# Kernel optimization log

Hardware: AMD Instinct MI355X
Metric: run time of the kernel (lower is better)

The kernel has to match this reference:

```python
import jax, jax.numpy as jnp
import numpy as np
import math

DIM = 1024
N_HEADS = 16
HEAD_DIM = DIM // N_HEADS


def get_sin_cos(seq_len, dim):
    # theta: (dim/2,), freqs: (L, dim/2), emb: (L, dim)
    theta = 10000.0 ** (-jnp.arange(0, dim, 2, dtype=jnp.float32) / dim)
    position = jnp.arange(seq_len, dtype=jnp.float32)
    freqs = position[:, None] * theta[None, :]
    emb = jnp.concatenate([jnp.sin(freqs), jnp.cos(freqs)], axis=-1)
    sin = emb[None, None]  # (1,1,L,dim)
    cos = emb[None, None]
    return sin, cos


def rotate_half(x):
    x1, x2 = x[..., ::2], x[..., 1::2]
    return jnp.concatenate([-x2, x1], axis=-1)


def apply_rope(q, k):
    sin, cos = get_sin_cos(q.shape[2], q.shape[-1])
    q = q * cos + rotate_half(q) * sin
    k = k * cos + rotate_half(k) * sin
    return q, k


def setup_inputs() -> dict:
    key = jax.random.key(0)
    ks = jax.random.split(key, 3)
    B, L, D = 2, 2048, DIM
    x = jax.random.normal(ks[0], (B, L, D), dtype=jnp.float32)
    Wqkv = jax.random.normal(ks[1], (D, 3 * D), dtype=jnp.float32) * (1.0 / math.sqrt(D))
    bqkv = jnp.zeros((3 * D,), dtype=jnp.float32)
    Wout = jax.random.normal(ks[2], (D, D), dtype=jnp.float32) * (1.0 / math.sqrt(D))
    bout = jnp.zeros((D,), dtype=jnp.float32)
    return {"x": x, "Wqkv": Wqkv, "bqkv": bqkv, "Wout": Wout, "bout": bout}


def reference(x, Wqkv, bqkv, Wout, bout):
    B, L, D = x.shape
    H, Hd = N_HEADS, HEAD_DIM
    qkv = (x @ Wqkv + bqkv).reshape(B, L, 3, H, Hd)
    q, k, v = qkv[:, :, 0], qkv[:, :, 1], qkv[:, :, 2]  # (B,L,H,Hd)
    q = q.transpose(0, 2, 1, 3)  # (B,H,L,Hd)
    k = k.transpose(0, 2, 1, 3)
    v = v.transpose(0, 2, 1, 3)
    q, k = apply_rope(q, k)
    scores = jnp.einsum('bhqd,bhkd->bhqk', q, k) / math.sqrt(Hd)
    probs = jax.nn.softmax(scores, axis=-1)
    out = jnp.einsum('bhqk,bhkd->bhqd', probs, v)
    out = out.transpose(0, 2, 1, 3).reshape(B, L, D)
    return out @ Wout + bout
```

## Files before the change

### kernel.cpp

```cpp
#include <hip/hip_runtime.h>
#include <hip/hip_bf16.h>
#include <math.h>

typedef __bf16 bf16;
typedef __bf16 bf16x8 __attribute__((ext_vector_type(8)));
typedef __bf16 bf16x4 __attribute__((ext_vector_type(4)));
typedef float f32x4 __attribute__((ext_vector_type(4)));
typedef float f32x16 __attribute__((ext_vector_type(16)));

#define DEV __device__ __forceinline__
#define AS1(p) ((const __attribute__((address_space(1))) void*)(p))
#define AS3(p) ((__attribute__((address_space(3))) void*)(p))

#define Bsz 2
#define Lseq 2048
#define Dm 1024
#define Hh 16
#define HD 64
#define BL (Bsz * Lseq)
#define TN (3 * Dm)

#define LOG2E 1.44269504088896f

#define OFF_XATT  ((size_t)0)
#define OFF_WQKVT (OFF_XATT  + (size_t)BL * Dm * 2)
#define OFF_WOUTT (OFF_WQKVT + (size_t)TN * Dm * 2)
#define OFF_TAB   (OFF_WOUTT + (size_t)Dm * Dm * 2)
#define OFF_Q     (OFF_TAB   + (size_t)Lseq * 32 * 8)
#define OFF_K     (OFF_Q     + (size_t)BL * Dm * 2)
#define OFF_VT    (OFF_K     + (size_t)BL * Dm * 2)

DEV float exp2_fast(float x) {
    float r;
    asm("v_exp_f32 %0, %1" : "=v"(r) : "v"(x));
    return r;
}

__global__ __launch_bounds__(256) void k_convert(const float* __restrict__ in,
                                                 bf16* __restrict__ out) {
    int i = blockIdx.x * 256 + threadIdx.x;
    const float4* in4 = (const float4*)in;
    float4 a = in4[i * 2];
    float4 b = in4[i * 2 + 1];
    bf16x8 o;
    o[0] = (bf16)a.x; o[1] = (bf16)a.y; o[2] = (bf16)a.z; o[3] = (bf16)a.w;
    o[4] = (bf16)b.x; o[5] = (bf16)b.y; o[6] = (bf16)b.z; o[7] = (bf16)b.w;
    ((bf16x8*)out)[i] = o;
}

__global__ __launch_bounds__(256) void k_transpose(const float* __restrict__ in,
                                                   bf16* __restrict__ out,
                                                   int R, int C) {
    __shared__ float t[32][33];
    int bx = blockIdx.x * 32;
    int by = blockIdx.y * 32;
    int tx = threadIdx.x, ty = threadIdx.y;
#pragma unroll
    for (int i = 0; i < 32; i += 8)
        t[ty + i][tx] = in[(size_t)(by + ty + i) * C + bx + tx];
    __syncthreads();
#pragma unroll
    for (int i = 0; i < 32; i += 8)
        out[(size_t)(bx + ty + i) * R + by + tx] = (bf16)t[tx][ty + i];
}

__global__ __launch_bounds__(256) void k_sincos(float2* __restrict__ tab) {
    int idx = blockIdx.x * 256 + threadIdx.x;
    int pos = idx >> 5, t = idx & 31;
    float theta = powf(10000.0f, -(float)t * (1.0f / 32.0f));
    float f = (float)pos * theta;
    tab[idx] = make_float2(sinf(f), cosf(f));
}

template <int EPI>
DEV void gemm_body(const bf16* __restrict__ A,
                   const bf16* __restrict__ BT,
                   const float* __restrict__ bias,
                   float* __restrict__ C,
                   bf16* __restrict__ qo,
                   bf16* __restrict__ ko,
                   bf16* __restrict__ vt,
                   const float2* __restrict__ tab,
                   int N, int K) {
    __shared__ uint4 smem4[2048];
    char* Al = (char*)smem4;
    char* Bl = (char*)smem4 + 16384;
    const int tid = threadIdx.x;
    const int w = tid >> 6, lane = tid & 63, lg = lane >> 4, lr = lane & 15;
    const int m0 = blockIdx.y * 128, n0 = blockIdx.x * 128;
    const int wm = (w >> 1) * 64, wn = (w & 1) * 64;
    const char* Ab = (const char*)A;
    const char* Bb = (const char*)BT;
    const size_t Kb = (size_t)K * 2;

    f32x4 acc[4][4] = {};

    const int rowL = lane >> 3;
    const int j16 = ((lane & 7) ^ rowL) * 16;

    for (int kt = 0; kt < K; kt += 64) {
#pragma unroll
        for (int c = 0; c < 4; ++c) {
            const int R0 = (w * 4 + c) * 8;
            const int row = R0 + rowL;
            __builtin_amdgcn_global_load_lds(AS1(Ab + (size_t)(m0 + row) * Kb + kt * 2 + j16),
                                             AS3(Al + R0 * 128), 16, 0, 0);
            __builtin_amdgcn_global_load_lds(AS1(Bb + (size_t)(n0 + row) * Kb + kt * 2 + j16),
                                             AS3(Bl + R0 * 128), 16, 0, 0);
        }
        __syncthreads();
#pragma unroll
        for (int kf = 0; kf < 2; ++kf) {
            bf16x8 af[4], bfr[4];
#pragma unroll
            for (int i = 0; i < 4; ++i) {
                int ra = wm + i * 16 + lr;
                af[i] = *(const bf16x8*)(Al + ra * 128 + ((kf * 64 + lg * 16) ^ ((ra & 7) << 4)));
                int rb = wn + i * 16 + lr;
                bfr[i] = *(const bf16x8*)(Bl + rb * 128 + ((kf * 64 + lg * 16) ^ ((rb & 7) << 4)));
            }
#pragma unroll
            for (int i = 0; i < 4; ++i)
#pragma unroll
                for (int j = 0; j < 4; ++j)
                    acc[i][j] = __builtin_amdgcn_mfma_f32_16x16x32_bf16(af[i], bfr[j], acc[i][j], 0, 0, 0);
        }
        __syncthreads();
    }

    if constexpr (EPI == 0) {
#pragma unroll
        for (int i = 0; i < 4; ++i) {
            int row = m0 + wm + i * 16 + lg * 4;
#pragma unroll
            for (int j = 0; j < 4; ++j) {
                int col = n0 + wn + j * 16 + lr;
                float bv = bias[col];
#pragma unroll
                for (int r = 0; r < 4; ++r)
                    C[(size_t)(row + r) * N + col] = acc[i][j][r] + bv;
            }
        }
    } else {
        const int phase = n0 >> 10;
        const int c0 = n0 + wn;
        const int h = (c0 & 1023) >> 6;
        const int b = m0 >> 11;
        const int bh = b * 16 + h;
        const int lbase = (m0 & 2047) + wm;
        float bv[4];
#pragma unroll
        for (int j = 0; j < 4; ++j) bv[j] = bias[c0 + j * 16 + lr];
        float* Lw = (float*)((char*)smem4 + w * 4096);

#pragma unroll
        for (int i = 0; i < 4; ++i) {
#pragma unroll
            for (int j = 0; j < 4; ++j)
#pragma unroll
                for (int r = 0; r < 4; ++r)
                    Lw[(lg * 4 + r) * 64 + j * 16 + lr] = acc[i][j][r] + bv[j];
            __syncthreads();
            if (phase < 2) {
                const float scale = (phase == 0) ? 0.125f * LOG2E : 1.0f;
                bf16* dst = (phase == 0 ? qo : ko) + (size_t)bh * Lseq * 64;
#pragma unroll
                for (int j = 0; j < 4; ++j)
#pragma unroll
                    for (int r = 0; r < 4; ++r) {
                        int rl = lg * 4 + r;
                        int d = j * 16 + lr;
                        int l = lbase + i * 16 + rl;
                        float v = Lw[rl * 64 + d];
                        int dp = (d < 32) ? (2 * d + 1) : (2 * d - 64);
                        float p = Lw[rl * 64 + dp];
                        float2 f = tab[l * 32 + (d & 31)];
                        float val = ((d < 32) ? (v - p) * f.x : (v + p) * f.y) * scale;
                        dst[(size_t)l * 64 + d] = (bf16)val;
                    }
            } else {
                int d = lane;
                int lb = lbase + i * 16;
                bf16x8 o1, o2;
#pragma unroll
                for (int rw = 0; rw < 8; ++rw) {
                    o1[rw] = (bf16)Lw[rw * 64 + d];
                    o2[rw] = (bf16)Lw[(rw + 8) * 64 + d];
                }
                bf16* dst = vt + ((size_t)bh * 64 + d) * Lseq + lb;
                *(bf16x8*)dst = o1;
                *(bf16x8*)(dst + 8) = o2;
            }
            __syncthreads();
        }
    }
}

__global__ __launch_bounds__(256) void k_gemm_qkv(const bf16* __restrict__ A,
                                                  const bf16* __restrict__ BT,
                                                  const float* __restrict__ bias,
                                                  bf16* __restrict__ qo,
                                                  bf16* __restrict__ ko,
                                                  bf16* __restrict__ vt,
                                                  const float2* __restrict__ tab) {
    gemm_body<1>(A, BT, bias, nullptr, qo, ko, vt, tab, TN, Dm);
}
__global__ __launch_bounds__(256) void k_gemm_out(const bf16* __restrict__ A,
                                                  const bf16* __restrict__ BT,
                                                  const float* __restrict__ bias,
                                                  float* __restrict__ C) {
    gemm_body<0>(A, BT, bias, C, nullptr, nullptr, nullptr, nullptr, Dm, Dm);
}

DEV f32x16 mfma32(bf16x8 a, bf16x8 b, f32x16 c) {
    return __builtin_amdgcn_mfma_f32_32x32x16_bf16(a, b, c, 0, 0, 0);
}
DEV unsigned packbf(float lo, float hi) {
    unsigned short a = __builtin_bit_cast(unsigned short, (bf16)lo);
    unsigned short b = __builtin_bit_cast(unsigned short, (bf16)hi);
    return (unsigned)a | ((unsigned)b << 16);
}

DEV void stage_tile(const char* kb, const char* vb, char* Kn, char* Vn,
                    int j0, int w, int lane) {
#pragma unroll
    for (int c = 0; c < 2; ++c) {
        const int j = w * 2 + c;
        const int rsw = lane ^ j;
        __builtin_amdgcn_global_load_lds(AS1(kb + (size_t)(j0 + rsw) * 128 + j * 16),
                                         AS3(Kn + j * 1024), 16, 0, 0);
        __builtin_amdgcn_global_load_lds(AS1(vb + (size_t)rsw * 4096 + (size_t)j0 * 2 + j * 16),
                                         AS3(Vn + j * 1024), 16, 0, 0);
    }
}

__global__ __launch_bounds__(256, 2) void k_attn(const bf16* __restrict__ Q,
                                                 const bf16* __restrict__ Kt,
                                                 const bf16* __restrict__ Vt,
                                                 bf16* __restrict__ Op) {
    __shared__ uint4 smem4[2048];
    char* base = (char*)smem4;
    const int tid = threadIdx.x;
    const int w = tid >> 6, lane = tid & 63;
    const int hi = lane >> 5, l31 = lane & 31;
    const int bid = blockIdx.x;
    const int bh = bid >> 4, qt = bid & 15;
    const int q0 = qt * 128 + w * 32;
    const char* qb = (const char*)(Q + (size_t)bh * Lseq * 64);
    const char* kb = (const char*)(Kt + (size_t)bh * Lseq * 64);
    const char* vb = (const char*)(Vt + (size_t)bh * 64 * Lseq);

    bf16x8 qf[4];
#pragma unroll
    for (int kst = 0; kst < 4; ++kst)
        qf[kst] = *(const bf16x8*)(qb + (size_t)(q0 + l31) * 128 + kst * 32 + hi * 16);

    f32x16 o0 = {}, o1 = {};
    float m = -1e30f, lsum = 0.f;

    stage_tile(kb, vb, base, base + 8192, 0, w, lane);
    __syncthreads();

    for (int jt = 0; jt < 32; ++jt) {
        const int cur = jt & 1;
        const char* Kl = base + cur * 16384;
        const char* Vl = Kl + 8192;
        char* Kn = base + (cur ^ 1) * 16384;
        char* Vn = Kn + 8192;

        if (jt < 31) stage_tile(kb, vb, Kn, Vn, (jt + 1) * 64, w, lane);

        f32x16 s0 = {}, s1 = {};
        __builtin_amdgcn_s_setprio(1);
#pragma unroll
        for (int kst = 0; kst < 4; ++kst) {
            const int jK = kst * 2 + hi;
            const int x = l31 ^ jK;
            bf16x8 ka = *(const bf16x8*)(Kl + jK * 1024 + x * 16);
            bf16x8 kc = *(const bf16x8*)(Kl + jK * 1024 + (32 + x) * 16);
            s0 = mfma32(ka, qf[kst], s0);
            s1 = mfma32(kc, qf[kst], s1);
        }
        __builtin_amdgcn_s_setprio(0);

        float pm = fmaxf(s0[0], s0[1]);
#pragma unroll
        for (int r = 2; r < 16; ++r) pm = fmaxf(pm, s0[r]);
#pragma unroll
        for (int r = 0; r < 16; ++r) pm = fmaxf(pm, s1[r]);
        pm = fmaxf(pm, __shfl_xor(pm, 32));
        if (!__all(pm <= m + 8.0f)) {
            float mn = fmaxf(m, pm);
            float sc = exp2_fast(m - mn);
#pragma unroll
            for (int r = 0; r < 16; ++r) { o0[r] *= sc; o1[r] *= sc; }
            lsum *= sc; m = mn;
        }
        float rs = 0.f;
#pragma unroll
        for (int r = 0; r < 16; ++r) { s0[r] = exp2_fast(s0[r] - m); rs += s0[r]; }
#pragma unroll
        for (int r = 0; r < 16; ++r) { s1[r] = exp2_fast(s1[r] - m); rs += s1[r]; }
        rs += __shfl_xor(rs, 32);
        lsum += rs;

        unsigned u[16];
#pragma unroll
        for (int t = 0; t < 8; ++t) {
            u[t]     = packbf(s0[2 * t], s0[2 * t + 1]);
            u[8 + t] = packbf(s1[2 * t], s1[2 * t + 1]);
        }
        unsigned snd[8], rcv[8];
#pragma unroll
        for (int J = 0; J < 2; ++J)
#pragma unroll
            for (int st = 0; st < 2; ++st) {
                const int t0 = J * 8 + st * 4, q = (J * 2 + st) * 2;
                snd[q + 0] = hi ? u[t0 + 0] : u[t0 + 2];
                snd[q + 1] = hi ? u[t0 + 1] : u[t0 + 3];
            }
#pragma unroll
        for (int t = 0; t < 8; ++t) rcv[t] = __shfl_xor(snd[t], 32);
        bf16x8 pf[2][2];
#pragma unroll
        for (int J = 0; J < 2; ++J)
#pragma unroll
            for (int st = 0; st < 2; ++st) {
                const int t0 = J * 8 + st * 4, q = (J * 2 + st) * 2;
                union { unsigned wd[4]; bf16x8 v; } f;
                f.wd[0] = hi ? rcv[q + 0] : u[t0 + 0];
                f.wd[1] = hi ? rcv[q + 1] : u[t0 + 1];
                f.wd[2] = hi ? u[t0 + 2] : rcv[q + 0];
                f.wd[3] = hi ? u[t0 + 3] : rcv[q + 1];
                pf[J][st] = f.v;
            }

        __builtin_amdgcn_s_setprio(1);
#pragma unroll
        for (int J = 0; J < 2; ++J)
#pragma unroll
            for (int st = 0; st < 2; ++st) {
                const int jV = J * 4 + st * 2 + hi;
                const int x = l31 ^ jV;
                bf16x8 v0 = *(const bf16x8*)(Vl + jV * 1024 + x * 16);
                bf16x8 v1 = *(const bf16x8*)(Vl + jV * 1024 + (32 + x) * 16);
                o0 = mfma32(v0, pf[J][st], o0);
                o1 = mfma32(v1, pf[J][st], o1);
            }
        __builtin_amdgcn_s_setprio(0);
        __syncthreads();
    }

    const float inv = 1.0f / lsum;
    const int b = bh >> 4, h = bh & 15;
    bf16* dst = Op + (size_t)(b * Lseq + q0 + l31) * Dm + h * 64;
#pragma unroll
    for (int t = 0; t < 4; ++t) {
        bf16x4 p0, p1;
#pragma unroll
        for (int i = 0; i < 4; ++i) {
            p0[i] = (bf16)(o0[4 * t + i] * inv);
            p1[i] = (bf16)(o1[4 * t + i] * inv);
        }
        *(bf16x4*)(dst + 8 * t + 4 * hi) = p0;
        *(bf16x4*)(dst + 32 + 8 * t + 4 * hi) = p1;
    }
}

extern "C" void kernel_launch(void* const* d_in, const int* in_sizes, int n_in,
                              void* d_out, int out_size, void* d_ws, size_t ws_size,
                              hipStream_t stream) {
    (void)in_sizes; (void)n_in; (void)out_size; (void)ws_size;
    const float* x    = (const float*)d_in[0];
    const float* Wqkv = (const float*)d_in[1];
    const float* bqkv = (const float*)d_in[2];
    const float* Wout = (const float*)d_in[3];
    const float* bout = (const float*)d_in[4];
    float* out = (float*)d_out;
    char* ws = (char*)d_ws;

    bf16* xbf    = (bf16*)(ws + OFF_XATT);
    bf16* att    = (bf16*)(ws + OFF_XATT);
    bf16* wqkvT  = (bf16*)(ws + OFF_WQKVT);
    bf16* woutT  = (bf16*)(ws + OFF_WOUTT);
    float2* tab  = (float2*)(ws + OFF_TAB);
    bf16* qb     = (bf16*)(ws + OFF_Q);
    bf16* kb     = (bf16*)(ws + OFF_K);
    bf16* vt     = (bf16*)(ws + OFF_VT);

    hipLaunchKernelGGL(k_convert, dim3((BL * Dm) / 8 / 256), dim3(256), 0, stream, x, xbf);
    hipLaunchKernelGGL(k_transpose, dim3(TN / 32, Dm / 32), dim3(32, 8), 0, stream, Wqkv, wqkvT, Dm, TN);
    hipLaunchKernelGGL(k_transpose, dim3(Dm / 32, Dm / 32), dim3(32, 8), 0, stream, Wout, woutT, Dm, Dm);
    hipLaunchKernelGGL(k_sincos, dim3(Lseq * 32 / 256), dim3(256), 0, stream, tab);
    hipLaunchKernelGGL(k_gemm_qkv, dim3(TN / 128, BL / 128), dim3(256), 0, stream,
                       xbf, wqkvT, bqkv, qb, kb, vt, tab);
    hipLaunchKernelGGL(k_attn, dim3(32 * 16), dim3(256), 0, stream, qb, kb, vt, att);
    hipLaunchKernelGGL(k_gemm_out, dim3(Dm / 128, BL / 128), dim3(256), 0, stream,
                       att, woutT, bout, out);
}
```

Before: 144.1 us.

## Split attention KV range across two wave groups per block and merge softmax

The attention block grows to 512 threads. Two sets of four waves each process half of the key/value sequence for the same 128 queries, and each set has its own double-buffered LDS region. At the end the partial outputs, maxima and sums are exchanged through LDS and merged flash-decoding style. This doubles the waves available to hide latency and halves the serial loop length per wave. The cost is doubled LDS use, a final reduction step, and fewer resident blocks per CU.

```diff
diff --git a/kernel.cpp b/kernel.cpp
--- a/kernel.cpp
+++ b/kernel.cpp
@@ -222,10 +222,10 @@
 }
 
 DEV void stage_tile(const char* kb, const char* vb, char* Kn, char* Vn,
-                    int j0, int w, int lane) {
+                    int j0, int qw, int lane) {
 #pragma unroll
     for (int c = 0; c < 2; ++c) {
-        const int j = w * 2 + c;
+        const int j = qw * 2 + c;
         const int rsw = lane ^ j;
         __builtin_amdgcn_global_load_lds(AS1(kb + (size_t)(j0 + rsw) * 128 + j * 16),
                                          AS3(Kn + j * 1024), 16, 0, 0);
@@ -234,21 +234,23 @@
     }
 }
 
-__global__ __launch_bounds__(256, 2) void k_attn(const bf16* __restrict__ Q,
+__global__ __launch_bounds__(512, 4) void k_attn(const bf16* __restrict__ Q,
                                                  const bf16* __restrict__ Kt,
                                                  const bf16* __restrict__ Vt,
                                                  bf16* __restrict__ Op) {
-    __shared__ uint4 smem4[2048];
+    __shared__ uint4 smem4[4096];
     char* base = (char*)smem4;
     const int tid = threadIdx.x;
     const int w = tid >> 6, lane = tid & 63;
+    const int qw = w & 3, s = w >> 2;
     const int hi = lane >> 5, l31 = lane & 31;
     const int bid = blockIdx.x;
     const int bh = bid >> 4, qt = bid & 15;
-    const int q0 = qt * 128 + w * 32;
+    const int q0 = qt * 128 + qw * 32;
     const char* qb = (const char*)(Q + (size_t)bh * Lseq * 64);
     const char* kb = (const char*)(Kt + (size_t)bh * Lseq * 64);
     const char* vb = (const char*)(Vt + (size_t)bh * 64 * Lseq);
+    char* setb = base + s * 32768;
 
     bf16x8 qf[4];
 #pragma unroll
@@ -258,17 +260,17 @@
     f32x16 o0 = {}, o1 = {};
     float m = -1e30f, lsum = 0.f;
 
-    stage_tile(kb, vb, base, base + 8192, 0, w, lane);
+    stage_tile(kb, vb, setb, setb + 8192, s * 16 * 64, qw, lane);
     __syncthreads();
 
-    for (int jt = 0; jt < 32; ++jt) {
-        const int cur = jt & 1;
-        const char* Kl = base + cur * 16384;
+    for (int t = 0; t < 16; ++t) {
+        const int cur = t & 1;
+        const char* Kl = setb + cur * 16384;
         const char* Vl = Kl + 8192;
-        char* Kn = base + (cur ^ 1) * 16384;
+        char* Kn = setb + (cur ^ 1) * 16384;
         char* Vn = Kn + 8192;
 
-        if (jt < 31) stage_tile(kb, vb, Kn, Vn, (jt + 1) * 64, w, lane);
+        if (t < 15) stage_tile(kb, vb, Kn, Vn, (s * 16 + t + 1) * 64, qw, lane);
 
         f32x16 s0 = {}, s1 = {};
         __builtin_amdgcn_s_setprio(1);
@@ -306,9 +308,9 @@
 
         unsigned u[16];
 #pragma unroll
-        for (int t = 0; t < 8; ++t) {
-            u[t]     = packbf(s0[2 * t], s0[2 * t + 1]);
-            u[8 + t] = packbf(s1[2 * t], s1[2 * t + 1]);
+        for (int t2 = 0; t2 < 8; ++t2) {
+            u[t2]     = packbf(s0[2 * t2], s0[2 * t2 + 1]);
+            u[8 + t2] = packbf(s1[2 * t2], s1[2 * t2 + 1]);
         }
         unsigned snd[8], rcv[8];
 #pragma unroll
@@ -320,7 +322,7 @@
                 snd[q + 1] = hi ? u[t0 + 1] : u[t0 + 3];
             }
 #pragma unroll
-        for (int t = 0; t < 8; ++t) rcv[t] = __shfl_xor(snd[t], 32);
+        for (int t2 = 0; t2 < 8; ++t2) rcv[t2] = __shfl_xor(snd[t2], 32);
         bf16x8 pf[2][2];
 #pragma unroll
         for (int J = 0; J < 2; ++J)
@@ -351,19 +353,38 @@
         __syncthreads();
     }
 
-    const float inv = 1.0f / lsum;
-    const int b = bh >> 4, h = bh & 15;
-    bf16* dst = Op + (size_t)(b * Lseq + q0 + l31) * Dm + h * 64;
-#pragma unroll
-    for (int t = 0; t < 4; ++t) {
-        bf16x4 p0, p1;
-#pragma unroll
-        for (int i = 0; i < 4; ++i) {
-            p0[i] = (bf16)(o0[4 * t + i] * inv);
-            p1[i] = (bf16)(o1[4 * t + i] * inv);
-        }
-        *(bf16x4*)(dst + 8 * t + 4 * hi) = p0;
-        *(bf16x4*)(dst + 32 + 8 * t + 4 * hi) = p1;
+    float* ex = (float*)base;
+    if (s == 1) {
+        float* r = ex + qw * 2176;
+#pragma unroll
+        for (int t = 0; t < 16; ++t) {
+            r[t * 64 + lane] = o0[t];
+            r[1024 + t * 64 + lane] = o1[t];
+        }
+        r[2048 + lane] = m;
+        r[2112 + lane] = lsum;
+    }
+    __syncthreads();
+    if (s == 0) {
+        float* r = ex + qw * 2176;
+        const float mb = r[2048 + lane], lb = r[2112 + lane];
+        const float M = fmaxf(m, mb);
+        const float wa = exp2_fast(m - M), wb = exp2_fast(mb - M);
+        const float inv = 1.0f / (wa * lsum + wb * lb);
+        const float fa = wa * inv, fb = wb * inv;
+        const int b = bh >> 4, h = bh & 15;
+        bf16* dst = Op + (size_t)(b * Lseq + q0 + l31) * Dm + h * 64;
+#pragma unroll
+        for (int t = 0; t < 4; ++t) {
+            bf16x4 p0, p1;
+#pragma unroll
+            for (int i = 0; i < 4; ++i) {
+                p0[i] = (bf16)(o0[4 * t + i] * fa + r[(4 * t + i) * 64 + lane] * fb);
+                p1[i] = (bf16)(o1[4 * t + i] * fa + r[1024 + (4 * t + i) * 64 + lane] * fb);
+            }
+            *(bf16x4*)(dst + 8 * t + 4 * hi) = p0;
+            *(bf16x4*)(dst + 32 + 8 * t + 4 * hi) = p1;
+        }
     }
 }
 
@@ -394,7 +415,7 @@
     hipLaunchKernelGGL(k_sincos, dim3(Lseq * 32 / 256), dim3(256), 0, stream, tab);
     hipLaunchKernelGGL(k_gemm_qkv, dim3(TN / 128, BL / 128), dim3(256), 0, stream,
                        xbf, wqkvT, bqkv, qb, kb, vt, tab);
-    hipLaunchKernelGGL(k_attn, dim3(32 * 16), dim3(256), 0, stream, qb, kb, vt, att);
+    hipLaunchKernelGGL(k_attn, dim3(32 * 16), dim3(512), 0, stream, qb, kb, vt, att);
     hipLaunchKernelGGL(k_gemm_out, dim3(Dm / 128, BL / 128), dim3(256), 0, stream,
                        att, woutT, bout, out);
 }
```

Result: no change. 141.9 us (-1.5%).
